# Kernel optimization log

Measured on AMD Instinct MI355X. Metric: run time of the kernel, lower is better.

The kernel has to match this reference:

```python
import jax, jax.numpy as jnp
import numpy as np
import math

B, H, L, D = 2, 16, 2048, 64
NEG_E = 1000000000000.0  # the module's default e


def setup_inputs() -> dict:
    key = jax.random.key(0)
    kq, kk, kv, km = jax.random.split(key, 4)
    q = jax.random.normal(kq, (B, H, L, D), dtype=jnp.float32)
    k = jax.random.normal(kk, (B, H, L, D), dtype=jnp.float32)
    v = jax.random.normal(kv, (B, H, L, D), dtype=jnp.float32)
    mask = jax.random.randint(km, (B, L, L), 0, 2, dtype=jnp.int32)
    return {"q": q, "k": k, "v": v, "mask": mask}


def reference(q, k, v, mask):
    b, h, l, d = k.shape
    # FAITHFUL quirk 1: original does k.view(B,H,D,L) -- a reshape, NOT a transpose.
    k_t = jnp.reshape(k, (b, h, d, l))
    score = jnp.matmul(q, k_t) / math.sqrt(d)  # [B,H,L,L]
    # mask.unsqueeze(1): broadcast over heads; masked positions -> -e
    score = jnp.where(mask[:, None, :, :] == 0, jnp.float32(-NEG_E), score)
    # FAITHFUL quirk 2: nn.Softmax(dim=1) normalizes over the HEAD axis.
    score = jax.nn.softmax(score, axis=1)
    out = jnp.matmul(score, v)  # [B,H,L,D]
    return (out, score)
```

## Files before the change

kernel.cpp:

```cpp
#include <hip/hip_runtime.h>
#include <math.h>

#define NB 2
#define NH 16
#define LSEQ 2048
#define DD 64
#define HSZ (LSEQ*DD)
#define NELEM (NB*NH*HSZ)
#define NSLICE 4

typedef _Float16 half_t;
typedef _Float16 f16x4 __attribute__((ext_vector_type(4)));
typedef _Float16 f16x8 __attribute__((ext_vector_type(8)));
typedef float    f32x4 __attribute__((ext_vector_type(4)));
typedef int      i32x4 __attribute__((ext_vector_type(4)));

__global__ __launch_bounds__(256) void convert_q(
    const float* __restrict__ q, half_t* __restrict__ qh)
{
    const int n4 = NELEM / 4;
    for (int gid = blockIdx.x * 256 + threadIdx.x; gid < n4; gid += gridDim.x * 256) {
        f32x4 x = __builtin_nontemporal_load((const f32x4*)q + gid);
        f16x4 y;
        y[0] = (half_t)x[0]; y[1] = (half_t)x[1]; y[2] = (half_t)x[2]; y[3] = (half_t)x[3];
        ((f16x4*)qh)[gid] = y;
    }
}

__global__ __launch_bounds__(256) void transpose_cvt(
    const float* __restrict__ k, const float* __restrict__ v,
    half_t* __restrict__ kt, half_t* __restrict__ vt)
{
    __shared__ half_t lds[64][72];
    const int tid = threadIdx.x;
    const int bh  = blockIdx.y;
    const int t64 = blockIdx.x;
    const float* src; half_t* dst; int C, R, r0, c0;
    if (blockIdx.z == 0) {
        src = k + (size_t)bh * HSZ; dst = kt + (size_t)bh * HSZ;
        R = 64; C = LSEQ; r0 = 0; c0 = t64 * 64;
    } else {
        src = v + (size_t)bh * HSZ; dst = vt + (size_t)bh * HSZ;
        R = LSEQ; C = 64; r0 = t64 * 64; c0 = 0;
    }
    const int rr = tid & 63, w4 = tid >> 6;
    #pragma unroll
    for (int qq = 0; qq < 4; ++qq) {
        f32x4 x = __builtin_nontemporal_load(
            (const f32x4*)&src[(size_t)(r0 + rr) * C + c0 + w4 * 16 + qq * 4]);
        lds[w4 * 16 + qq * 4 + 0][rr] = (half_t)x[0];
        lds[w4 * 16 + qq * 4 + 1][rr] = (half_t)x[1];
        lds[w4 * 16 + qq * 4 + 2][rr] = (half_t)x[2];
        lds[w4 * 16 + qq * 4 + 3][rr] = (half_t)x[3];
    }
    __syncthreads();
    #pragma unroll
    for (int p = 0; p < 2; ++p) {
        const int id = tid + p * 256;
        const int cl = id >> 3, rc = id & 7;
        f16x8 y = *(const f16x8*)&lds[cl][rc * 8];
        *(f16x8*)&dst[(size_t)(c0 + cl) * R + r0 + rc * 8] = y;
    }
}

__global__ __launch_bounds__(256, 4) void fused_attn_part(
    const half_t* __restrict__ qh, const half_t* __restrict__ kt,
    const half_t* __restrict__ vt, const int* __restrict__ mask,
    float* __restrict__ score, float* __restrict__ pout)
{
    __shared__ char smem_raw[35840];
    float*  red  = (float*)smem_raw;
    half_t* pbuf = (half_t*)(smem_raw + 17408);
    const int tid = threadIdx.x, w = tid >> 6, lane = tid & 63;
    const int n16 = lane & 15, g = lane >> 4;
    const int g4 = g * 4, g8 = g * 8;

    const int bid = blockIdx.x;
    const int xcd = bid & 7;
    const int b      = xcd >> 2;
    const int jslice = xcd & 3;
    const int i0 = (bid >> 3) * 16;
    const int t0 = jslice * 16;

    const size_t hb0 = (size_t)b * NH;
    const int h0 = w * 4;
    const int irow = i0 + n16;

    f16x8 qf[4][2];
    #pragma unroll
    for (int hh = 0; hh < 4; ++hh)
        #pragma unroll
        for (int kg = 0; kg < 2; ++kg)
            qf[hh][kg] = *(const f16x8*)(qh + (hb0 + h0 + hh) * (size_t)HSZ
                                         + (size_t)irow * DD + kg * 32 + g8);

    f32x4 acc[4][4];
    #pragma unroll
    for (int hh = 0; hh < 4; ++hh)
        #pragma unroll
        for (int ds = 0; ds < 4; ++ds) { acc[hh][ds][0]=0.f; acc[hh][ds][1]=0.f; acc[hh][ds][2]=0.f; acc[hh][ds][3]=0.f; }

    const int* mrow = mask + ((size_t)b * LSEQ + irow) * LSEQ;

    for (int t = t0; t < t0 + 16; ++t) {
        const int j0 = t * 32;
        i32x4 m0 = __builtin_nontemporal_load((const i32x4*)(mrow + j0 + g4));
        i32x4 m1 = __builtin_nontemporal_load((const i32x4*)(mrow + j0 + 16 + g4));
        int mvv[2][4] = {{m0[0], m0[1], m0[2], m0[3]}, {m1[0], m1[1], m1[2], m1[3]}};

        f32x4 sc[4][2];
        #pragma unroll
        for (int hh = 0; hh < 4; ++hh) {
            const half_t* kp = kt + (hb0 + h0 + hh) * (size_t)HSZ;
            #pragma unroll
            for (int jb = 0; jb < 2; ++jb) {
                const half_t* kr = kp + (size_t)(j0 + jb * 16 + n16) * DD;
                f16x8 k0 = *(const f16x8*)(kr + g8);
                f16x8 k1 = *(const f16x8*)(kr + 32 + g8);
                f32x4 c = {0.f, 0.f, 0.f, 0.f};
                c = __builtin_amdgcn_mfma_f32_16x16x32_f16(k0, qf[hh][0], c, 0, 0, 0);
                c = __builtin_amdgcn_mfma_f32_16x16x32_f16(k1, qf[hh][1], c, 0, 0, 0);
                sc[hh][jb] = c;
            }
        }

        f32x4 ps[2] = {{0.f,0.f,0.f,0.f}, {0.f,0.f,0.f,0.f}};
        #pragma unroll
        for (int hh = 0; hh < 4; ++hh)
            #pragma unroll
            for (int jb = 0; jb < 2; ++jb)
                #pragma unroll
                for (int r = 0; r < 4; ++r) {
                    float e = (mvv[jb][r] == 0) ? 1.0f : __expf(0.125f * sc[hh][jb][r]);
                    sc[hh][jb][r] = e;
                    ps[jb][r] += e;
                }

        float* rb = red + (t & 1) * 2176;
        #pragma unroll
        for (int jb = 0; jb < 2; ++jb)
            #pragma unroll
            for (int r = 0; r < 4; ++r)
                rb[((jb * 16 + g4 + r) * 4 + w) * 17 + n16] = ps[jb][r];
        asm volatile("s_waitcnt lgkmcnt(0)" ::: "memory");
        __builtin_amdgcn_s_barrier();

        float inv_[2][4];
        #pragma unroll
        for (int jb = 0; jb < 2; ++jb)
            #pragma unroll
            for (int r = 0; r < 4; ++r) {
                const int jc = (jb * 16 + g4 + r) * 4;
                float s = rb[(jc + 0) * 17 + n16] + rb[(jc + 1) * 17 + n16]
                        + rb[(jc + 2) * 17 + n16] + rb[(jc + 3) * 17 + n16];
                inv_[jb][r] = 1.0f / s;
            }

        #pragma unroll
        for (int hh = 0; hh < 4; ++hh) {
            half_t* pb_head = pbuf + (size_t)(w * 4 + hh) * 16 * 36;
            const half_t* vp = vt + (hb0 + h0 + hh) * (size_t)HSZ;
            #pragma unroll
            for (int jb = 0; jb < 2; ++jb) {
                f16x4 pb;
                #pragma unroll
                for (int r = 0; r < 4; ++r) pb[r] = (half_t)(sc[hh][jb][r] * inv_[jb][r]);
                *(f16x4*)(pb_head + n16 * 36 + jb * 16 + g4) = pb;
                #pragma unroll
                for (int ds = 0; ds < 4; ++ds) {
                    f16x4 av = *(const f16x4*)(vp + (size_t)(ds * 16 + n16) * LSEQ + j0 + jb * 16 + g4);
                    acc[hh][ds] = __builtin_amdgcn_mfma_f32_16x16x16f16(av, pb, acc[hh][ds], 0, 0, 0);
                }
            }
        }

        const int srow_ = lane >> 3, scol = (lane & 7) * 4;
        #pragma unroll
        for (int hh = 0; hh < 4; ++hh) {
            const half_t* pb_head = pbuf + (size_t)(w * 4 + hh) * 16 * 36;
            float* sbase = score + ((hb0 + h0 + hh) * LSEQ + i0) * LSEQ + j0;
            #pragma unroll
            for (int half_i = 0; half_i < 2; ++half_i) {
                const int row = half_i * 8 + srow_;
                f16x4 x = *(const f16x4*)(pb_head + row * 36 + scol);
                f32x4 y;
                y[0] = (float)x[0]; y[1] = (float)x[1]; y[2] = (float)x[2]; y[3] = (float)x[3];
                __builtin_nontemporal_store(y, (f32x4*)(sbase + (size_t)row * LSEQ + scol));
            }
        }
    }

    __syncthreads();
    float* pbase = pout + (size_t)jslice * NELEM;
    float* ep = (float*)smem_raw + w * 1088;
    const int erow = lane >> 4, ecol = (lane & 15) * 4;
    #pragma unroll
    for (int hh = 0; hh < 4; ++hh) {
        #pragma unroll
        for (int ds = 0; ds < 4; ++ds)
            *(f32x4*)&ep[n16 * 68 + ds * 16 + g4] = acc[hh][ds];
        asm volatile("s_waitcnt lgkmcnt(0)" ::: "memory");
        float* obase = pbase + (hb0 + h0 + hh) * (size_t)HSZ + (size_t)i0 * DD;
        #pragma unroll
        for (int qq = 0; qq < 4; ++qq) {
            const int row = qq * 4 + erow;
            f32x4 x = *(const f32x4*)&ep[row * 68 + ecol];
            __builtin_nontemporal_store(x, (f32x4*)(obase + (size_t)row * DD + ecol));
        }
        asm volatile("s_waitcnt lgkmcnt(0)" ::: "memory");
    }
}

__global__ __launch_bounds__(256) void reduce_out(
    const float* __restrict__ pout, float* __restrict__ out)
{
    const int n4 = NELEM / 4;
    for (int i = blockIdx.x * 256 + threadIdx.x; i < n4; i += gridDim.x * 256) {
        f32x4 a = __builtin_nontemporal_load((const f32x4*)pout + i);
        f32x4 bb = __builtin_nontemporal_load((const f32x4*)(pout + NELEM) + i);
        f32x4 c = __builtin_nontemporal_load((const f32x4*)(pout + 2 * (size_t)NELEM) + i);
        f32x4 d = __builtin_nontemporal_load((const f32x4*)(pout + 3 * (size_t)NELEM) + i);
        __builtin_nontemporal_store(a + bb + c + d, (f32x4*)out + i);
    }
}

extern "C" void kernel_launch(void* const* d_in, const int* in_sizes, int n_in,
                              void* d_out, int out_size, void* d_ws, size_t ws_size,
                              hipStream_t stream) {
    const float* q    = (const float*)d_in[0];
    const float* k    = (const float*)d_in[1];
    const float* v    = (const float*)d_in[2];
    const int*   mask = (const int*)d_in[3];

    float* out   = (float*)d_out;
    float* score = out + (size_t)NB * NH * LSEQ * DD;

    half_t* qh   = (half_t*)d_ws;
    half_t* kt   = qh + NELEM;
    half_t* vt   = kt + NELEM;
    float*  pout = (float*)(vt + NELEM);

    convert_q<<<2048, 256, 0, stream>>>(q, qh);
    transpose_cvt<<<dim3(32, NB * NH, 2), 256, 0, stream>>>(k, v, kt, vt);
    fused_attn_part<<<1024, 256, 0, stream>>>(qh, kt, vt, mask, score, pout);
    reduce_out<<<1024, 256, 0, stream>>>(pout, out);
}
```

Measured before the change: 570.5 us.

## Use 512-thread blocks covering 32 rows and a K=32 MFMA for the PV product

Each block now has 8 waves in two groups of four, covering 32 query rows instead of 16, so the grid halves. The reduction buffer is split per row group instead of double-buffered by iteration, which needs an extra barrier per step. The normalized probabilities are first written to LDS and read back as 8-wide fragments, so the PV product can use the 16x16x32 f16 MFMA in place of two 16x16x16 calls. This cuts MFMA issue count and lets both row groups share cached K/V lines, at the cost of more LDS, an extra barrier per iteration, and an aggressive launch bound that may limit registers.

```diff
diff --git a/kernel.cpp b/kernel.cpp
--- a/kernel.cpp
+++ b/kernel.cpp
@@ -14,6 +14,10 @@
 typedef _Float16 f16x8 __attribute__((ext_vector_type(8)));
 typedef float    f32x4 __attribute__((ext_vector_type(4)));
 typedef int      i32x4 __attribute__((ext_vector_type(4)));
+
+#define LGKM_BAR() do { \
+    asm volatile("s_waitcnt lgkmcnt(0)" ::: "memory"); \
+    __builtin_amdgcn_s_barrier(); } while (0)
 
 __global__ __launch_bounds__(256) void convert_q(
     const float* __restrict__ q, half_t* __restrict__ qh)
@@ -63,28 +67,29 @@
     }
 }
 
-__global__ __launch_bounds__(256, 4) void fused_attn_part(
+__global__ __launch_bounds__(512, 6) void fused_attn_part(
     const half_t* __restrict__ qh, const half_t* __restrict__ kt,
     const half_t* __restrict__ vt, const int* __restrict__ mask,
     float* __restrict__ score, float* __restrict__ pout)
 {
-    __shared__ char smem_raw[35840];
+    __shared__ char smem_raw[50176];
     float*  red  = (float*)smem_raw;
     half_t* pbuf = (half_t*)(smem_raw + 17408);
     const int tid = threadIdx.x, w = tid >> 6, lane = tid & 63;
     const int n16 = lane & 15, g = lane >> 4;
     const int g4 = g * 4, g8 = g * 8;
+    const int wl = w & 3, gi = w >> 2;
 
     const int bid = blockIdx.x;
     const int xcd = bid & 7;
     const int b      = xcd >> 2;
     const int jslice = xcd & 3;
-    const int i0 = (bid >> 3) * 16;
+    const int i0 = (bid >> 3) * 32;
     const int t0 = jslice * 16;
 
     const size_t hb0 = (size_t)b * NH;
-    const int h0 = w * 4;
-    const int irow = i0 + n16;
+    const int h0 = wl * 4;
+    const int irow = i0 + gi * 16 + n16;
 
     f16x8 qf[4][2];
     #pragma unroll
@@ -101,6 +106,7 @@
         for (int ds = 0; ds < 4; ++ds) { acc[hh][ds][0]=0.f; acc[hh][ds][1]=0.f; acc[hh][ds][2]=0.f; acc[hh][ds][3]=0.f; }
 
     const int* mrow = mask + ((size_t)b * LSEQ + irow) * LSEQ;
+    float* rb = red + gi * 2176;
 
     for (int t = t0; t < t0 + 16; ++t) {
         const int j0 = t * 32;
@@ -136,14 +142,12 @@
                     ps[jb][r] += e;
                 }
 
-        float* rb = red + (t & 1) * 2176;
         #pragma unroll
         for (int jb = 0; jb < 2; ++jb)
             #pragma unroll
             for (int r = 0; r < 4; ++r)
-                rb[((jb * 16 + g4 + r) * 4 + w) * 17 + n16] = ps[jb][r];
-        asm volatile("s_waitcnt lgkmcnt(0)" ::: "memory");
-        __builtin_amdgcn_s_barrier();
+                rb[((jb * 16 + g4 + r) * 4 + wl) * 17 + n16] = ps[jb][r];
+        LGKM_BAR();
 
         float inv_[2][4];
         #pragma unroll
@@ -155,34 +159,40 @@
                         + rb[(jc + 2) * 17 + n16] + rb[(jc + 3) * 17 + n16];
                 inv_[jb][r] = 1.0f / s;
             }
-
-        #pragma unroll
-        for (int hh = 0; hh < 4; ++hh) {
-            half_t* pb_head = pbuf + (size_t)(w * 4 + hh) * 16 * 36;
-            const half_t* vp = vt + (hb0 + h0 + hh) * (size_t)HSZ;
+        LGKM_BAR();
+
+        #pragma unroll
+        for (int hh = 0; hh < 4; ++hh) {
+            half_t* pb_head = pbuf + (size_t)(w * 4 + hh) * 512;
             #pragma unroll
             for (int jb = 0; jb < 2; ++jb) {
                 f16x4 pb;
                 #pragma unroll
                 for (int r = 0; r < 4; ++r) pb[r] = (half_t)(sc[hh][jb][r] * inv_[jb][r]);
-                *(f16x4*)(pb_head + n16 * 36 + jb * 16 + g4) = pb;
-                #pragma unroll
-                for (int ds = 0; ds < 4; ++ds) {
-                    f16x4 av = *(const f16x4*)(vp + (size_t)(ds * 16 + n16) * LSEQ + j0 + jb * 16 + g4);
-                    acc[hh][ds] = __builtin_amdgcn_mfma_f32_16x16x16f16(av, pb, acc[hh][ds], 0, 0, 0);
-                }
+                *(f16x4*)(pb_head + n16 * 32 + jb * 16 + g4) = pb;
+            }
+        }
+        #pragma unroll
+        for (int hh = 0; hh < 4; ++hh) {
+            const half_t* pb_head = pbuf + (size_t)(w * 4 + hh) * 512;
+            const half_t* vp = vt + (hb0 + h0 + hh) * (size_t)HSZ;
+            f16x8 pb8 = *(const f16x8*)(pb_head + n16 * 32 + g8);
+            #pragma unroll
+            for (int ds = 0; ds < 4; ++ds) {
+                f16x8 av8 = *(const f16x8*)(vp + (size_t)(ds * 16 + n16) * LSEQ + j0 + g8);
+                acc[hh][ds] = __builtin_amdgcn_mfma_f32_16x16x32_f16(av8, pb8, acc[hh][ds], 0, 0, 0);
             }
         }
 
         const int srow_ = lane >> 3, scol = (lane & 7) * 4;
         #pragma unroll
         for (int hh = 0; hh < 4; ++hh) {
-            const half_t* pb_head = pbuf + (size_t)(w * 4 + hh) * 16 * 36;
-            float* sbase = score + ((hb0 + h0 + hh) * LSEQ + i0) * LSEQ + j0;
+            const half_t* pb_head = pbuf + (size_t)(w * 4 + hh) * 512;
+            float* sbase = score + ((hb0 + h0 + hh) * LSEQ + i0 + gi * 16) * LSEQ + j0;
             #pragma unroll
             for (int half_i = 0; half_i < 2; ++half_i) {
                 const int row = half_i * 8 + srow_;
-                f16x4 x = *(const f16x4*)(pb_head + row * 36 + scol);
+                f16x4 x = *(const f16x4*)(pb_head + row * 32 + scol);
                 f32x4 y;
                 y[0] = (float)x[0]; y[1] = (float)x[1]; y[2] = (float)x[2]; y[3] = (float)x[3];
                 __builtin_nontemporal_store(y, (f32x4*)(sbase + (size_t)row * LSEQ + scol));
@@ -200,7 +210,7 @@
         for (int ds = 0; ds < 4; ++ds)
             *(f32x4*)&ep[n16 * 68 + ds * 16 + g4] = acc[hh][ds];
         asm volatile("s_waitcnt lgkmcnt(0)" ::: "memory");
-        float* obase = pbase + (hb0 + h0 + hh) * (size_t)HSZ + (size_t)i0 * DD;
+        float* obase = pbase + (hb0 + h0 + hh) * (size_t)HSZ + (size_t)(i0 + gi * 16) * DD;
         #pragma unroll
         for (int qq = 0; qq < 4; ++qq) {
             const int row = qq * 4 + erow;
@@ -242,6 +252,6 @@
 
     convert_q<<<2048, 256, 0, stream>>>(q, qh);
     transpose_cvt<<<dim3(32, NB * NH, 2), 256, 0, stream>>>(k, v, kt, vt);
-    fused_attn_part<<<1024, 256, 0, stream>>>(qh, kt, vt, mask, score, pout);
+    fused_attn_part<<<512, 512, 0, stream>>>(qh, kt, vt, mask, score, pout);
     reduce_out<<<1024, 256, 0, stream>>>(pout, out);
 }
```

Measured after the change: 723.9 us. 26.9% more time.
